# Kernel optimization log

Hardware: AMD Instinct MI355X
Metric: run time of the kernel (lower is better)

## Reference

```python
import jax, jax.numpy as jnp
import numpy as np

EPS = 1e-5
SLOPE = 0.2


def setup_inputs() -> dict:
    key = jax.random.key(0)
    ks = jax.random.split(key, 8)
    B, D, N = 8, 60, 1024
    dims = [(64, 120), (64, 64), (128, 64), (256, 128), (256, 512), (1024, 256)]
    inp = {"x": jax.random.normal(ks[0], (B, D, N), dtype=jnp.float32)}
    for i, (o, c) in enumerate(dims, 1):
        inp[f"w{i}"] = jax.random.normal(ks[i], (o, c), dtype=jnp.float32) / np.sqrt(c).astype(np.float32)
        inp[f"b{i}"] = jnp.zeros((o,), jnp.float32)
        inp[f"g{i}"] = jnp.ones((o,), jnp.float32)
        inp[f"be{i}"] = jnp.zeros((o,), jnp.float32)
    inp["k"] = 20
    return inp


def knn_idx(x, k):
    # x: [B, D, N] -> idx [B, N, k] of nearest neighbors (negative sq dist topk)
    inner = -2.0 * jnp.einsum('bdn,bdm->bnm', x, x)
    xx = jnp.sum(x * x, axis=1)  # [B, N]
    pd = -xx[:, :, None] - inner - xx[:, None, :]
    _, idx = jax.lax.top_k(pd, k)
    return idx


def get_graph_feature(x, k):
    # x: [B, D, N] -> [B, 2D, N, k]
    B, D, N = x.shape
    idx = knn_idx(x, k)  # [B, N, k]
    xt = jnp.transpose(x, (0, 2, 1))  # [B, N, D]
    nbr = xt[jnp.arange(B)[:, None, None], idx]  # [B, N, k, D]
    ctr = xt[:, :, None, :]  # [B, N, 1, D]
    feat = jnp.concatenate([nbr - ctr, jnp.broadcast_to(ctr, nbr.shape)], axis=-1)
    return jnp.transpose(feat, (0, 3, 1, 2))  # [B, 2D, N, k]


def lrelu(x):
    return jnp.where(x >= 0, x, SLOPE * x)


def bn(x, g, b, axes):
    # training-mode batch norm (biased variance), channel axis = 1
    m = jnp.mean(x, axis=axes, keepdims=True)
    v = jnp.mean((x - m) ** 2, axis=axes, keepdims=True)
    sh = [1] * x.ndim
    sh[1] = -1
    return (x - m) * jax.lax.rsqrt(v + EPS) * g.reshape(sh) + b.reshape(sh)


def conv2d1x1(x, w, b):
    return jnp.einsum('bcnk,oc->bonk', x, w) + b[None, :, None, None]


def conv1d1x1(x, w, b):
    return jnp.einsum('bcn,oc->bon', x, w) + b[None, :, None]


def reference(x, w1, b1, g1, be1, w2, b2, g2, be2, w3, b3, g3, be3,
              w4, b4, g4, be4, w5, b5, g5, be5, w6, b6, g6, be6, k):
    h = get_graph_feature(x, k)                             # [B,120,N,k]
    h = lrelu(bn(conv2d1x1(h, w1, b1), g1, be1, (0, 2, 3)))
    x1 = jnp.max(h, axis=-1)
    h = lrelu(bn(conv2d1x1(h, w2, b2), g2, be2, (0, 2, 3)))
    x2 = jnp.max(h, axis=-1)
    h = lrelu(bn(conv2d1x1(h, w3, b3), g3, be3, (0, 2, 3)))
    x3 = jnp.max(h, axis=-1)
    h = lrelu(bn(conv2d1x1(h, w4, b4), g4, be4, (0, 2, 3)))
    x4 = jnp.max(h, axis=-1)
    h = jnp.concatenate([x1, x2, x3, x4], axis=1)           # [B,512,N]
    h = lrelu(bn(conv1d1x1(h, w5, b5), g5, be5, (0, 2)))
    h = lrelu(bn(conv1d1x1(h, w6, b6), g6, be6, (0, 2)))
    return jnp.transpose(h, (0, 2, 1))                      # [B,N,emb_dims]
```

## Files before the change

### kernel.cpp

```cpp
#include <hip/hip_runtime.h>
#include <hip/hip_bf16.h>
#include <math.h>

#define B_ 8
#define D_ 60
#define N_ 1024
#define K_ 20
#define P1_ 8192
#define P2_ 163840

typedef __attribute__((ext_vector_type(8))) short bf16x8;
typedef __attribute__((ext_vector_type(4))) short bf16x4;
typedef __attribute__((ext_vector_type(4))) float f32x4;

__device__ inline float b2f(short s) { return __uint_as_float(((unsigned)(unsigned short)s) << 16); }
__device__ inline short f2b(float f) { __hip_bfloat16 h = __float2bfloat16(f); return *(short*)&h; }
__device__ inline unsigned fenc(float f) { unsigned b = __float_as_uint(f); return (b & 0x80000000u) ? ~b : (b | 0x80000000u); }
__device__ inline float fdec(unsigned k) { return __uint_as_float((k & 0x80000000u) ? (k ^ 0x80000000u) : ~k); }

#define OFF_IDX   0ull
#define OFF_XX    655360ull
#define OFF_STATS 688128ull
#define OFF_XT    720896ull
#define OFF_WB    1769472ull
#define OFF_XC    2662400ull
#define OFF_H5    11051008ull
#define OFF_H6    15245312ull
#define OFF_UV    32022528ull
#define OFF_XR1   36216832ull
#define OFF_XR2   38313984ull
#define OFF_XR3   40411136ull
#define OFF_XR4   44605440ull
#define OFF_H1    52994048ull
#define OFF_H2    73965568ull
#define OFF_H3    94937088ull
#define OFF_PART  136880128ull
#define OFF_PART2 139501568ull

#define WO1 0
#define WO2 8192
#define WO3 12288
#define WO4 20480
#define WO5 53248
#define WO6 184320

#define SO1 0
#define SO2 64
#define SO3 128
#define SO4 256
#define SO5 512
#define SO6 768
#define NCH_TOT 1792

__global__ __launch_bounds__(256) void k_xx(const float* __restrict__ x,
                                            float* __restrict__ xx) {
  int bn = blockIdx.x * 256 + threadIdx.x;
  int b = bn >> 10, n = bn & 1023;
  const float* xb = x + (size_t)b * D_ * N_ + n;
  float s = 0.f;
  for (int d = 0; d < D_; ++d) { float v = xb[(size_t)d * N_]; s += v * v; }
  xx[bn] = s;
}

__global__ __launch_bounds__(256) void k_pd(const float* __restrict__ x,
                                            const float* __restrict__ xx,
                                            float* __restrict__ pd) {
  __shared__ float lnn[D_][64];
  __shared__ float lmm[D_][128];
  int tid = threadIdx.x;
  int m0 = blockIdx.x * 128, n0 = blockIdx.y * 64, b = blockIdx.z;
  const float* xb = x + (size_t)b * D_ * N_;
  #pragma unroll
  for (int i = 0; i < 15; ++i) {
    int idx = tid + i * 256;
    int d = idx >> 6, col = idx & 63;
    lnn[d][col] = xb[(size_t)d * N_ + n0 + col];
  }
  #pragma unroll
  for (int i = 0; i < 30; ++i) {
    int idx = tid + i * 256;
    int d = idx >> 7, col = idx & 127;
    lmm[d][col] = xb[(size_t)d * N_ + m0 + col];
  }
  __syncthreads();
  int tn = tid >> 5, tm = tid & 31;
  float acc[8][4];
  #pragma unroll
  for (int i = 0; i < 8; ++i)
    #pragma unroll
    for (int j = 0; j < 4; ++j) acc[i][j] = 0.f;
  for (int d = 0; d < D_; ++d) {
    f32x4 mv  = *(const f32x4*)&lmm[d][tm * 4];
    f32x4 nva = *(const f32x4*)&lnn[d][tn * 8];
    f32x4 nvb = *(const f32x4*)&lnn[d][tn * 8 + 4];
    #pragma unroll
    for (int i = 0; i < 4; ++i)
      #pragma unroll
      for (int j = 0; j < 4; ++j) {
        acc[i][j]     = fmaf(nva[i], mv[j], acc[i][j]);
        acc[4 + i][j] = fmaf(nvb[i], mv[j], acc[4 + i][j]);
      }
  }
  const float* xxb = xx + b * 1024;
  f32x4 xxm = *(const f32x4*)(xxb + m0 + tm * 4);
  #pragma unroll
  for (int i = 0; i < 8; ++i) {
    int n = n0 + tn * 8 + i;
    float xxn = xxb[n];
    f32x4 o;
    #pragma unroll
    for (int j = 0; j < 4; ++j) o[j] = 2.f * acc[i][j] - xxn - xxm[j];
    *(f32x4*)(pd + ((size_t)(b * 1024 + n) * 1024) + m0 + tm * 4) = o;
  }
}

__global__ __launch_bounds__(256) void k_sel(const float* __restrict__ pd,
                                             int* __restrict__ idxb) {
  int tid = threadIdx.x;
  int wave = tid >> 6, lane = tid & 63;
  int bn = blockIdx.x * 4 + wave;
  const float* row = pd + (size_t)bn * 1024;
  int mbase = lane * 16;
  f32x4 r0 = *(const f32x4*)(row + mbase);
  f32x4 r1 = *(const f32x4*)(row + mbase + 4);
  f32x4 r2 = *(const f32x4*)(row + mbase + 8);
  f32x4 r3 = *(const f32x4*)(row + mbase + 12);
  float v[16];
  #pragma unroll
  for (int j = 0; j < 4; ++j) { v[j] = r0[j]; v[4 + j] = r1[j]; v[8 + j] = r2[j]; v[12 + j] = r3[j]; }
  int* outp = idxb + (size_t)bn * K_;
  for (int kk = 0; kk < K_; ++kk) {
    float bv = v[0]; int bj = 0;
    #pragma unroll
    for (int j = 1; j < 16; ++j)
      if (v[j] > bv) { bv = v[j]; bj = j; }
    int bi = mbase + bj;
    #pragma unroll
    for (int off = 1; off < 64; off <<= 1) {
      float ov = __shfl_xor(bv, off);
      int   oi = __shfl_xor(bi, off);
      if (ov > bv || (ov == bv && oi < bi)) { bv = ov; bi = oi; }
    }
    if (lane == 0) outp[kk] = bi;
    #pragma unroll
    for (int j = 0; j < 16; ++j)
      if (bi == mbase + j) v[j] = -INFINITY;
  }
}

__global__ __launch_bounds__(256) void k_xt(const float* __restrict__ x,
                                            short* __restrict__ xt) {
  int bn = blockIdx.x * 256 + threadIdx.x;
  int b = bn >> 10, n = bn & 1023;
  const float* xb = x + (size_t)b * D_ * N_ + n;
  short* row = xt + (size_t)bn * 64;
  for (int c = 0; c < 60; ++c) row[c] = f2b(xb[(size_t)c * N_]);
  row[60] = 0; row[61] = 0; row[62] = 0; row[63] = 0;
}

__global__ __launch_bounds__(256) void k_wuv(const float* __restrict__ w1,
                                             const float* __restrict__ b1,
                                             short* __restrict__ wuv,
                                             float* __restrict__ buv) {
  int t = blockIdx.x * 256 + threadIdx.x;
  int o = t >> 6, c = t & 63;
  float v = 0.f;
  if (o < 64) { if (c < 60) v = w1[o * 120 + c]; }
  else { int o2 = o - 64; if (c < 60) v = w1[o2 * 120 + 60 + c] - w1[o2 * 120 + c]; }
  wuv[t] = f2b(v);
  if (t < 128) buv[t] = (t < 64) ? 0.f : b1[t - 64];
}

__global__ __launch_bounds__(256) void k_wcvt(const float* __restrict__ w2,
                                              const float* __restrict__ w3,
                                              const float* __restrict__ w4,
                                              const float* __restrict__ w5,
                                              const float* __restrict__ w6,
                                              short* __restrict__ wbase) {
  int t = blockIdx.x * 256 + threadIdx.x;
  if (t < 4096) wbase[WO2 + t] = f2b(w2[t]);
  else if (t < 12288) wbase[WO3 + (t - 4096)] = f2b(w3[t - 4096]);
  else if (t < 45056) wbase[WO4 + (t - 12288)] = f2b(w4[t - 12288]);
  else if (t < 176128) wbase[WO5 + (t - 45056)] = f2b(w5[t - 45056]);
  else if (t < 438272) wbase[WO6 + (t - 176128)] = f2b(w6[t - 176128]);
}

template <int K, int COUT, bool APPLY, bool STATS, bool WMAX, bool HSTORE, bool F32OUT>
__global__ __launch_bounds__(256) void k_gemm(const short* __restrict__ in,
                                              const short* __restrict__ wb,
                                              const float* __restrict__ bias,
                                              const float* __restrict__ Ain,
                                              const float* __restrict__ Bin,
                                              float* __restrict__ part,
                                              short* __restrict__ out,
                                              unsigned* __restrict__ umax) {
  constexpr int KT = K / 32;
  constexpr int NX = COUT / 64;
  constexpr int MSZ = WMAX ? 128 * 68 : 4;
  __shared__ __align__(16) float m32s[MSZ];
  __shared__ float ls[128];
  int tid = threadIdx.x;
  int w = tid >> 6, lane = tid & 63;
  int ln = lane & 15, quad = lane >> 4;
  int bid = blockIdx.y * NX + blockIdx.x;
  int tot = NX * gridDim.y;
  int gid = (bid & 7) * (tot >> 3) + (bid >> 3);
  int bxx = gid % NX;
  int rp = gid / NX;
  int co0 = bxx * 64;
  const short* pA0 = in + ((size_t)(rp * 128 + w * 32 + ln)) * K + quad * 8;
  const short* pA1 = pA0 + (size_t)16 * K;
  const short* pW  = wb + ((size_t)(co0 + ln)) * K + quad * 8;

  f32x4 acc[4][2];
  #pragma unroll
  for (int m = 0; m < 4; ++m)
    #pragma unroll
    for (int t = 0; t < 2; ++t) acc[m][t] = (f32x4){0.f, 0.f, 0.f, 0.f};

  auto applyv = [&](bf16x8 v, int kc) -> bf16x8 {
    f32x4 a0 = *(const f32x4*)(Ain + kc);
    f32x4 a1 = *(const f32x4*)(Ain + kc + 4);
    f32x4 b0 = *(const f32x4*)(Bin + kc);
    f32x4 b1 = *(const f32x4*)(Bin + kc + 4);
    #pragma unroll
    for (int j = 0; j < 8; ++j) {
      float aj = j < 4 ? a0[j] : a1[j - 4];
      float bj = j < 4 ? b0[j] : b1[j - 4];
      float f = b2f(v[j]) * aj + bj;
      f = f >= 0.f ? f : 0.2f * f;
      v[j] = f2b(f);
    }
    return v;
  };

  bf16x8 wf0[4], wf1[4], af0[2], af1[2];
  #pragma unroll
  for (int m = 0; m < 4; ++m) wf0[m] = *(const bf16x8*)(pW + (size_t)m * 16 * K);
  af0[0] = *(const bf16x8*)(pA0);
  af0[1] = *(const bf16x8*)(pA1);
  if (APPLY) { af0[0] = applyv(af0[0], quad * 8); af0[1] = applyv(af0[1], quad * 8); }

  for (int kt = 0; kt < KT; kt += 2) {
    {
      int off = (kt + 1) * 32;
      #pragma unroll
      for (int m = 0; m < 4; ++m) wf1[m] = *(const bf16x8*)(pW + (size_t)m * 16 * K + off);
      af1[0] = *(const bf16x8*)(pA0 + off);
      af1[1] = *(const bf16x8*)(pA1 + off);
      if (APPLY) { af1[0] = applyv(af1[0], off + quad * 8); af1[1] = applyv(af1[1], off + quad * 8); }
    }
    #pragma unroll
    for (int m = 0; m < 4; ++m) {
      acc[m][0] = __builtin_amdgcn_mfma_f32_16x16x32_bf16(wf0[m], af0[0], acc[m][0], 0, 0, 0);
      acc[m][1] = __builtin_amdgcn_mfma_f32_16x16x32_bf16(wf0[m], af0[1], acc[m][1], 0, 0, 0);
    }
    if (kt + 2 < KT) {
      int off = (kt + 2) * 32;
      #pragma unroll
      for (int m = 0; m < 4; ++m) wf0[m] = *(const bf16x8*)(pW + (size_t)m * 16 * K + off);
      af0[0] = *(const bf16x8*)(pA0 + off);
      af0[1] = *(const bf16x8*)(pA1 + off);
      if (APPLY) { af0[0] = applyv(af0[0], off + quad * 8); af0[1] = applyv(af0[1], off + quad * 8); }
    }
    #pragma unroll
    for (int m = 0; m < 4; ++m) {
      acc[m][0] = __builtin_amdgcn_mfma_f32_16x16x32_bf16(wf1[m], af1[0], acc[m][0], 0, 0, 0);
      acc[m][1] = __builtin_amdgcn_mfma_f32_16x16x32_bf16(wf1[m], af1[1], acc[m][1], 0, 0, 0);
    }
  }

  #pragma unroll
  for (int m = 0; m < 4; ++m) {
    f32x4 bs = *(const f32x4*)(bias + co0 + m * 16 + quad * 4);
    #pragma unroll
    for (int t = 0; t < 2; ++t)
      #pragma unroll
      for (int r = 0; r < 4; ++r) acc[m][t][r] += bs[r];
  }
  if (HSTORE) {
    #pragma unroll
    for (int m = 0; m < 4; ++m)
      #pragma unroll
      for (int t = 0; t < 2; ++t) {
        int p = rp * 128 + w * 32 + t * 16 + ln;
        if (F32OUT) {
          *(f32x4*)((float*)out + (size_t)p * COUT + co0 + m * 16 + quad * 4) = acc[m][t];
        } else {
          bf16x4 o;
          #pragma unroll
          for (int r = 0; r < 4; ++r) o[r] = f2b(acc[m][t][r]);
          *(bf16x4*)(out + (size_t)p * COUT + co0 + m * 16 + quad * 4) = o;
        }
      }
  }
  if (STATS || WMAX) {
    if (STATS && tid < 128) ls[tid] = 0.f;
    if (WMAX) {
      #pragma unroll
      for (int m = 0; m < 4; ++m)
        #pragma unroll
        for (int t = 0; t < 2; ++t)
          *(f32x4*)(m32s + (size_t)(w * 32 + t * 16 + ln) * 68 + m * 16 + quad * 4) = acc[m][t];
    }
    __syncthreads();
    if (STATS) {
      #pragma unroll
      for (int m = 0; m < 4; ++m)
        #pragma unroll
        for (int r = 0; r < 4; ++r) {
          float v0 = acc[m][0][r], v1 = acc[m][1][r];
          float s = v0 + v1, ss = v0 * v0 + v1 * v1;
          #pragma unroll
          for (int off = 1; off < 16; off <<= 1) {
            s += __shfl_xor(s, off); ss += __shfl_xor(ss, off);
          }
          if (ln == 0) {
            atomicAdd(&ls[m * 16 + quad * 4 + r], s);
            atomicAdd(&ls[64 + m * 16 + quad * 4 + r], ss);
          }
        }
    }
    if (WMAX) {
      int r0 = rp * 128;
      int pt0 = r0 / 20;
      int npt = (r0 + 127) / 20 - pt0 + 1;
      if (tid < npt * 16) {
        int lpt = tid >> 4, cq = (tid & 15) * 4;
        int ptg = pt0 + lpt;
        int rs = ptg * 20 - r0, re = rs + 20;
        rs = rs < 0 ? 0 : rs;
        re = re > 128 ? 128 : re;
        f32x4 mv = (f32x4){-INFINITY, -INFINITY, -INFINITY, -INFINITY};
        for (int r = rs; r < re; ++r) {
          f32x4 v = *(const f32x4*)(m32s + (size_t)r * 68 + cq);
          #pragma unroll
          for (int j = 0; j < 4; ++j) mv[j] = fmaxf(mv[j], v[j]);
        }
        #pragma unroll
        for (int j = 0; j < 4; ++j)
          atomicMax(&umax[(size_t)ptg * COUT + co0 + cq + j], fenc(mv[j]));
      }
    }
  }
  if (STATS) {
    __syncthreads();
    if (tid < 128)
      part[((size_t)bxx * gridDim.y + rp) * 128 + tid] = ls[tid];
  }
}

__global__ __launch_bounds__(256) void k_expand(const float* __restrict__ UVf,
                                                const int* __restrict__ idxb,
                                                short* __restrict__ h1,
                                                float* __restrict__ xr1,
                                                float* __restrict__ part) {
  int tid = threadIdx.x;
  int lp = tid >> 4;
  int c0 = (tid & 15) * 4;
  int pt = blockIdx.x * 16 + lp;
  int base = (pt >> 10) << 10;
  f32x4 V = *(const f32x4*)(UVf + (size_t)pt * 128 + 64 + c0);
  f32x4 sum = (f32x4){0.f, 0.f, 0.f, 0.f};
  f32x4 ssq = (f32x4){0.f, 0.f, 0.f, 0.f};
  f32x4 mx = (f32x4){-INFINITY, -INFINITY, -INFINITY, -INFINITY};
  const int* ip = idxb + (size_t)pt * K_;
  size_t hb = (size_t)pt * K_ * 64 + c0;
  for (int k = 0; k < K_; ++k) {
    int nb = base + ip[k];
    f32x4 U = *(const f32x4*)(UVf + (size_t)nb * 128 + c0);
    bf16x4 o;
    #pragma unroll
    for (int j = 0; j < 4; ++j) {
      float h = U[j] + V[j];
      mx[j] = fmaxf(mx[j], U[j]);
      sum[j] += h; ssq[j] += h * h;
      o[j] = f2b(h);
    }
    *(bf16x4*)(h1 + hb + (size_t)k * 64) = o;
  }
  f32x4 xo;
  #pragma unroll
  for (int j = 0; j < 4; ++j) xo[j] = mx[j] + V[j];
  *(f32x4*)(xr1 + (size_t)pt * 64 + c0) = xo;
  __shared__ float ls[2048];
  *(f32x4*)(ls + tid * 4) = sum;
  *(f32x4*)(ls + 1024 + tid * 4) = ssq;
  __syncthreads();
  if (tid < 32) {
    int cl = tid & 15;
    bool issq = tid >= 16;
    const float* src = ls + (issq ? 1024 : 0);
    f32x4 s = (f32x4){0.f, 0.f, 0.f, 0.f};
    #pragma unroll
    for (int g = 0; g < 16; ++g) {
      f32x4 v = *(const f32x4*)(src + (g * 16 + cl) * 4);
      s[0] += v[0]; s[1] += v[1]; s[2] += v[2]; s[3] += v[3];
    }
    *(f32x4*)(part + (size_t)blockIdx.x * 128 + (issq ? 64 : 0) + cl * 4) = s;
  }
}

__global__ __launch_bounds__(256) void k_red(const float* __restrict__ part, int NB,
                                             float* __restrict__ part2) {
  int cc = blockIdx.x, by = blockIdx.y;
  int tid = threadIdx.x;
  int rg = tid >> 5;
  int c4 = (tid & 31) * 4;
  int chunk = NB >> 5;
  const float* p = part + ((size_t)cc * NB + (size_t)by * chunk) * 128;
  f32x4 acc = (f32x4){0.f, 0.f, 0.f, 0.f};
  for (int r = rg; r < chunk; r += 8) {
    f32x4 v = *(const f32x4*)(p + (size_t)r * 128 + c4);
    acc[0] += v[0]; acc[1] += v[1]; acc[2] += v[2]; acc[3] += v[3];
  }
  __shared__ float lds[1024];
  *(f32x4*)(lds + tid * 4) = acc;
  __syncthreads();
  if (tid < 32) {
    f32x4 s = (f32x4){0.f, 0.f, 0.f, 0.f};
    #pragma unroll
    for (int g = 0; g < 8; ++g) {
      f32x4 v = *(const f32x4*)(lds + (g * 32 + tid) * 4);
      s[0] += v[0]; s[1] += v[1]; s[2] += v[2]; s[3] += v[3];
    }
    *(f32x4*)(part2 + ((size_t)cc * 32 + by) * 128 + tid * 4) = s;
  }
}

__global__ __launch_bounds__(256) void k_bnab(const float* __restrict__ part, int NB,
                                              const float* __restrict__ g,
                                              const float* __restrict__ be,
                                              float* __restrict__ A,
                                              float* __restrict__ Bp, float inv) {
  __shared__ float red[256];
  int tid = threadIdx.x;
  int j = tid & 127, h = tid >> 7;
  const float* p = part + (size_t)blockIdx.x * NB * 128;
  float s = 0.f;
  for (int bx = h; bx < NB; bx += 2) s += p[(size_t)bx * 128 + j];
  red[tid] = s;
  __syncthreads();
  if (tid < 128) red[tid] = red[tid] + red[tid + 128];
  __syncthreads();
  if (tid < 64) {
    int c = blockIdx.x * 64 + tid;
    float m = red[tid] * inv;
    float v = red[64 + tid] * inv - m * m;
    float a = g[c] * rsqrtf(v + 1e-5f);
    A[c] = a; Bp[c] = be[c] - m * a;
  }
}

__global__ __launch_bounds__(256) void k_xcat(const float* __restrict__ xr1,
                                              const unsigned* __restrict__ xr2,
                                              const unsigned* __restrict__ xr3,
                                              const unsigned* __restrict__ xr4,
                                              const float* __restrict__ A,
                                              const float* __restrict__ Bp,
                                              short* __restrict__ xcat) {
  int t = blockIdx.x * 256 + threadIdx.x;
  int p = t >> 7, cq = t & 127;
  int c0 = cq * 4;
  f32x4 v;
  if (c0 < 64) {
    v = *(const f32x4*)(xr1 + (size_t)p * 64 + c0);
  } else {
    const unsigned* src; int cc;
    if (c0 < 128)      { src = xr2 + (size_t)p * 64;  cc = c0 - 64; }
    else if (c0 < 256) { src = xr3 + (size_t)p * 128; cc = c0 - 128; }
    else               { src = xr4 + (size_t)p * 256; cc = c0 - 256; }
    #pragma unroll
    for (int j = 0; j < 4; ++j) v[j] = fdec(src[cc + j]);
  }
  f32x4 a = *(const f32x4*)(A + c0);
  f32x4 b = *(const f32x4*)(Bp + c0);
  bf16x4 o;
  #pragma unroll
  for (int j = 0; j < 4; ++j) {
    float f = v[j] * a[j] + b[j];
    f = f >= 0.f ? f : 0.2f * f;
    o[j] = f2b(f);
  }
  *(bf16x4*)(xcat + (size_t)p * 512 + c0) = o;
}

__global__ __launch_bounds__(256) void k_apply_out(const short* __restrict__ h,
                                                   const float* __restrict__ A,
                                                   const float* __restrict__ Bp,
                                                   float* __restrict__ out) {
  int t = blockIdx.x * 256 + threadIdx.x;
  int c0 = (t & 255) * 4;
  f32x4 a = *(const f32x4*)(A + c0);
  f32x4 b = *(const f32x4*)(Bp + c0);
  bf16x4 v = *(const bf16x4*)(h + (size_t)t * 4);
  f32x4 o;
  #pragma unroll
  for (int r = 0; r < 4; ++r) {
    float f = b2f(v[r]) * a[r] + b[r];
    o[r] = f >= 0.f ? f : 0.2f * f;
  }
  *(f32x4*)(out + (size_t)t * 4) = o;
}

extern "C" void kernel_launch(void* const* d_in, const int* in_sizes, int n_in,
                              void* d_out, int out_size, void* d_ws, size_t ws_size,
                              hipStream_t stream) {
  const float* x   = (const float*)d_in[0];
  const float* w1  = (const float*)d_in[1];
  const float* b1  = (const float*)d_in[2];
  const float* g1  = (const float*)d_in[3];
  const float* be1 = (const float*)d_in[4];
  const float* w2  = (const float*)d_in[5];
  const float* b2  = (const float*)d_in[6];
  const float* g2  = (const float*)d_in[7];
  const float* be2 = (const float*)d_in[8];
  const float* w3  = (const float*)d_in[9];
  const float* b3  = (const float*)d_in[10];
  const float* g3  = (const float*)d_in[11];
  const float* be3 = (const float*)d_in[12];
  const float* w4  = (const float*)d_in[13];
  const float* b4  = (const float*)d_in[14];
  const float* g4  = (const float*)d_in[15];
  const float* be4 = (const float*)d_in[16];
  const float* w5  = (const float*)d_in[17];
  const float* b5  = (const float*)d_in[18];
  const float* g5  = (const float*)d_in[19];
  const float* be5 = (const float*)d_in[20];
  const float* w6  = (const float*)d_in[21];
  const float* b6  = (const float*)d_in[22];
  const float* g6  = (const float*)d_in[23];
  const float* be6 = (const float*)d_in[24];
  float* out = (float*)d_out;
  char* ws = (char*)d_ws;

  int*      idxb = (int*)(ws + OFF_IDX);
  float*    xx   = (float*)(ws + OFF_XX);
  float*    Aall = (float*)(ws + OFF_STATS);
  float*    Ball = Aall + NCH_TOT;
  float*    buv  = Ball + NCH_TOT;
  short*    xt   = (short*)(ws + OFF_XT);
  short*    wbb  = (short*)(ws + OFF_WB);
  short*    xcat = (short*)(ws + OFF_XC);
  short*    h5   = (short*)(ws + OFF_H5);
  short*    h6   = (short*)(ws + OFF_H6);
  float*    UVf  = (float*)(ws + OFF_UV);
  float*    xr1  = (float*)(ws + OFF_XR1);
  unsigned* xr2  = (unsigned*)(ws + OFF_XR2);
  unsigned* xr3  = (unsigned*)(ws + OFF_XR3);
  unsigned* xr4  = (unsigned*)(ws + OFF_XR4);
  short*    h1   = (short*)(ws + OFF_H1);
  short*    h2   = (short*)(ws + OFF_H2);
  short*    h3   = (short*)(ws + OFF_H3);
  float*    pd    = (float*)(ws + OFF_H3);
  float*    part  = (float*)(ws + OFF_PART);
  float*    part2 = (float*)(ws + OFF_PART2);

  hipMemsetAsync(ws + OFF_XR2, 0, 2097152ull + 4194304ull + 8388608ull, stream);

  k_xx <<<P1_ / 256, 256, 0, stream>>>(x, xx);
  k_pd <<<dim3(8, 16, 8), 256, 0, stream>>>(x, xx, pd);
  k_sel<<<P1_ / 4, 256, 0, stream>>>(pd, idxb);
  k_xt <<<P1_ / 256, 256, 0, stream>>>(x, xt);
  k_wuv<<<32, 256, 0, stream>>>(w1, b1, wbb + WO1, buv);
  k_wcvt<<<1712, 256, 0, stream>>>(w2, w3, w4, w5, w6, wbb);

  k_gemm<64, 128, false, false, false, true, true><<<dim3(2, 64), 256, 0, stream>>>(
      xt, wbb + WO1, buv, nullptr, nullptr, nullptr, (short*)UVf, nullptr);
  k_expand<<<P1_ / 16, 256, 0, stream>>>(UVf, idxb, h1, xr1, part);
  k_red <<<dim3(1, 32), 256, 0, stream>>>(part, P1_ / 16, part2);
  k_bnab<<<1, 256, 0, stream>>>(part2, 32, g1, be1, Aall + SO1, Ball + SO1, 1.f / P2_);

  k_gemm<64, 64, true, true, true, true, false><<<dim3(1, P2_ / 128), 256, 0, stream>>>(
      h1, wbb + WO2, b2, Aall + SO1, Ball + SO1, part, h2, xr2);
  k_red <<<dim3(1, 32), 256, 0, stream>>>(part, P2_ / 128, part2);
  k_bnab<<<1, 256, 0, stream>>>(part2, 32, g2, be2, Aall + SO2, Ball + SO2, 1.f / P2_);

  k_gemm<64, 128, true, true, true, true, false><<<dim3(2, P2_ / 128), 256, 0, stream>>>(
      h2, wbb + WO3, b3, Aall + SO2, Ball + SO2, part, h3, xr3);
  k_red <<<dim3(2, 32), 256, 0, stream>>>(part, P2_ / 128, part2);
  k_bnab<<<2, 256, 0, stream>>>(part2, 32, g3, be3, Aall + SO3, Ball + SO3, 1.f / P2_);

  k_gemm<128, 256, true, true, true, false, false><<<dim3(4, P2_ / 128), 256, 0, stream>>>(
      h3, wbb + WO4, b4, Aall + SO3, Ball + SO3, part, nullptr, xr4);
  k_red <<<dim3(4, 32), 256, 0, stream>>>(part, P2_ / 128, part2);
  k_bnab<<<4, 256, 0, stream>>>(part2, 32, g4, be4, Aall + SO4, Ball + SO4, 1.f / P2_);

  k_xcat<<<P1_ * 128 / 256, 256, 0, stream>>>(xr1, xr2, xr3, xr4, Aall, Ball, xcat);

  k_gemm<512, 256, false, true, false, true, false><<<dim3(4, P1_ / 128), 256, 0, stream>>>(
      xcat, wbb + WO5, b5, nullptr, nullptr, part, h5, nullptr);
  k_bnab<<<4, 256, 0, stream>>>(part, P1_ / 128, g5, be5, Aall + SO5, Ball + SO5, 1.f / P1_);

  k_gemm<256, 1024, true, true, false, true, false><<<dim3(16, P1_ / 128), 256, 0, stream>>>(
      h5, wbb + WO6, b6, Aall + SO5, Ball + SO5, part, h6, nullptr);
  k_bnab<<<16, 256, 0, stream>>>(part, P1_ / 128, g6, be6, Aall + SO6, Ball + SO6, 1.f / P1_);
  k_apply_out<<<P1_ * 256 / 256, 256, 0, stream>>>(h6, Aall + SO6, Ball + SO6, out);

  (void)in_sizes; (void)n_in; (void)out_size; (void)ws_size;
}
```

Before: 477.6 us.

## Stage GEMM tiles through swizzled LDS with async global_load_lds double buffering

Rewrites the MFMA GEMM so operand tiles are copied into XOR-swizzled shared memory with global_load_lds and double buffered. Each block now handles several 128-row tiles (NR) to amortise weight loads and launch count. Per-channel stats are reduced with wave shuffles and written per wave instead of through shared-memory atomics. The neighbour max is done with shuffle-based segmented reduction and global atomicMax instead of a shared-memory staging buffer. This changes the partial-sum counts and the workspace offset, and it adds a barrier on every K-step.

```diff
diff --git a/kernel.cpp b/kernel.cpp
--- a/kernel.cpp
+++ b/kernel.cpp
@@ -17,6 +17,12 @@
 __device__ inline short f2b(float f) { __hip_bfloat16 h = __float2bfloat16(f); return *(short*)&h; }
 __device__ inline unsigned fenc(float f) { unsigned b = __float_as_uint(f); return (b & 0x80000000u) ? ~b : (b | 0x80000000u); }
 __device__ inline float fdec(unsigned k) { return __uint_as_float((k & 0x80000000u) ? (k ^ 0x80000000u) : ~k); }
+
+__device__ __forceinline__ void gl16(const short* g, short* l) {
+  __builtin_amdgcn_global_load_lds(
+      (const __attribute__((address_space(1))) unsigned int*)g,
+      (__attribute__((address_space(3))) unsigned int*)l, 16, 0, 0);
+}
 
 #define OFF_IDX   0ull
 #define OFF_XX    655360ull
@@ -35,7 +41,7 @@
 #define OFF_H2    73965568ull
 #define OFF_H3    94937088ull
 #define OFF_PART  136880128ull
-#define OFF_PART2 139501568ull
+#define OFF_PART2 149463040ull
 
 #define WO1 0
 #define WO2 8192
@@ -185,7 +191,7 @@
   else if (t < 438272) wbase[WO6 + (t - 176128)] = f2b(w6[t - 176128]);
 }
 
-template <int K, int COUT, bool APPLY, bool STATS, bool WMAX, bool HSTORE, bool F32OUT>
+template <int K, int COUT, int NR, bool APPLY, bool STATS, bool WMAX, bool HSTORE, bool F32OUT>
 __global__ __launch_bounds__(256) void k_gemm(const short* __restrict__ in,
                                               const short* __restrict__ wb,
                                               const float* __restrict__ bias,
@@ -194,29 +200,43 @@
                                               float* __restrict__ part,
                                               short* __restrict__ out,
                                               unsigned* __restrict__ umax) {
-  constexpr int KT = K / 32;
-  constexpr int NX = COUT / 64;
-  constexpr int MSZ = WMAX ? 128 * 68 : 4;
-  __shared__ __align__(16) float m32s[MSZ];
-  __shared__ float ls[128];
+  constexpr int NKP = K / 64;
+  constexpr int NP  = NR * NKP;
+  constexpr int ASZ = 128 * 64;
+  constexpr int WSZ = 64 * 64;
+  __shared__ __align__(16) short ldsA[2 * ASZ];
+  __shared__ __align__(16) short ldsW[2 * WSZ];
+
   int tid = threadIdx.x;
   int w = tid >> 6, lane = tid & 63;
   int ln = lane & 15, quad = lane >> 4;
-  int bid = blockIdx.y * NX + blockIdx.x;
-  int tot = NX * gridDim.y;
+  int xsl = ln & 7;
+  int bid = blockIdx.y * gridDim.x + blockIdx.x;
+  int tot = gridDim.x * gridDim.y;
   int gid = (bid & 7) * (tot >> 3) + (bid >> 3);
-  int bxx = gid % NX;
-  int rp = gid / NX;
+  int bxx = gid % gridDim.x;
+  int rpB = gid / gridDim.x;
   int co0 = bxx * 64;
-  const short* pA0 = in + ((size_t)(rp * 128 + w * 32 + ln)) * K + quad * 8;
-  const short* pA1 = pA0 + (size_t)16 * K;
-  const short* pW  = wb + ((size_t)(co0 + ln)) * K + quad * 8;
-
-  f32x4 acc[4][2];
-  #pragma unroll
-  for (int m = 0; m < 4; ++m)
-    #pragma unroll
-    for (int t = 0; t < 2; ++t) acc[m][t] = (f32x4){0.f, 0.f, 0.f, 0.f};
+
+  const int rl = lane >> 3;
+  const int c16 = (lane & 7) ^ (rl & 7);
+
+  auto stage = [&](int p, int b) {
+    const int rp_ = rpB * NR + p / NKP;
+    const int kp_ = p % NKP;
+    const short* sA = in + (size_t)(rp_ * 128) * K + kp_ * 64;
+    #pragma unroll
+    for (int i = 0; i < 4; ++i) {
+      int ch = w * 4 + i;
+      gl16(sA + (size_t)(ch * 8 + rl) * K + c16 * 8, ldsA + b * ASZ + ch * 512);
+    }
+    const short* sW = wb + (size_t)co0 * K + kp_ * 64;
+    #pragma unroll
+    for (int i = 0; i < 2; ++i) {
+      int ch = w * 2 + i;
+      gl16(sW + (size_t)(ch * 8 + rl) * K + c16 * 8, ldsW + b * WSZ + ch * 512);
+    }
+  };
 
   auto applyv = [&](bf16x8 v, int kc) -> bf16x8 {
     f32x4 a0 = *(const f32x4*)(Ain + kc);
@@ -234,119 +254,120 @@
     return v;
   };
 
-  bf16x8 wf0[4], wf1[4], af0[2], af1[2];
-  #pragma unroll
-  for (int m = 0; m < 4; ++m) wf0[m] = *(const bf16x8*)(pW + (size_t)m * 16 * K);
-  af0[0] = *(const bf16x8*)(pA0);
-  af0[1] = *(const bf16x8*)(pA1);
-  if (APPLY) { af0[0] = applyv(af0[0], quad * 8); af0[1] = applyv(af0[1], quad * 8); }
-
-  for (int kt = 0; kt < KT; kt += 2) {
-    {
-      int off = (kt + 1) * 32;
+  f32x4 acc[4][2];
+  float sacc[4][4], ssacc[4][4];
+  #pragma unroll
+  for (int m = 0; m < 4; ++m)
+    #pragma unroll
+    for (int j = 0; j < 4; ++j) { sacc[m][j] = 0.f; ssacc[m][j] = 0.f; }
+
+  stage(0, 0);
+  __syncthreads();
+
+  for (int p = 0; p < NP; ++p) {
+    const int b = p & 1;
+    if (p + 1 < NP) stage(p + 1, b ^ 1);
+    const int rp_ = rpB * NR + p / NKP;
+    const int kp_ = p % NKP;
+    if (kp_ == 0) {
       #pragma unroll
-      for (int m = 0; m < 4; ++m) wf1[m] = *(const bf16x8*)(pW + (size_t)m * 16 * K + off);
-      af1[0] = *(const bf16x8*)(pA0 + off);
-      af1[1] = *(const bf16x8*)(pA1 + off);
-      if (APPLY) { af1[0] = applyv(af1[0], off + quad * 8); af1[1] = applyv(af1[1], off + quad * 8); }
-    }
-    #pragma unroll
-    for (int m = 0; m < 4; ++m) {
-      acc[m][0] = __builtin_amdgcn_mfma_f32_16x16x32_bf16(wf0[m], af0[0], acc[m][0], 0, 0, 0);
-      acc[m][1] = __builtin_amdgcn_mfma_f32_16x16x32_bf16(wf0[m], af0[1], acc[m][1], 0, 0, 0);
-    }
-    if (kt + 2 < KT) {
-      int off = (kt + 2) * 32;
+      for (int m = 0; m < 4; ++m)
+        #pragma unroll
+        for (int t = 0; t < 2; ++t) acc[m][t] = (f32x4){0.f, 0.f, 0.f, 0.f};
+    }
+    #pragma unroll
+    for (int ks = 0; ks < 2; ++ks) {
+      bf16x8 fw[4], fa[2];
+      int sl = ((ks * 4 + quad) ^ xsl) * 8;
       #pragma unroll
-      for (int m = 0; m < 4; ++m) wf0[m] = *(const bf16x8*)(pW + (size_t)m * 16 * K + off);
-      af0[0] = *(const bf16x8*)(pA0 + off);
-      af0[1] = *(const bf16x8*)(pA1 + off);
-      if (APPLY) { af0[0] = applyv(af0[0], off + quad * 8); af0[1] = applyv(af0[1], off + quad * 8); }
-    }
-    #pragma unroll
-    for (int m = 0; m < 4; ++m) {
-      acc[m][0] = __builtin_amdgcn_mfma_f32_16x16x32_bf16(wf1[m], af1[0], acc[m][0], 0, 0, 0);
-      acc[m][1] = __builtin_amdgcn_mfma_f32_16x16x32_bf16(wf1[m], af1[1], acc[m][1], 0, 0, 0);
-    }
-  }
-
-  #pragma unroll
-  for (int m = 0; m < 4; ++m) {
-    f32x4 bs = *(const f32x4*)(bias + co0 + m * 16 + quad * 4);
-    #pragma unroll
-    for (int t = 0; t < 2; ++t)
-      #pragma unroll
-      for (int r = 0; r < 4; ++r) acc[m][t][r] += bs[r];
-  }
-  if (HSTORE) {
-    #pragma unroll
-    for (int m = 0; m < 4; ++m)
+      for (int m = 0; m < 4; ++m)
+        fw[m] = *(const bf16x8*)(ldsW + b * WSZ + (m * 16 + ln) * 64 + sl);
       #pragma unroll
       for (int t = 0; t < 2; ++t) {
-        int p = rp * 128 + w * 32 + t * 16 + ln;
-        if (F32OUT) {
-          *(f32x4*)((float*)out + (size_t)p * COUT + co0 + m * 16 + quad * 4) = acc[m][t];
-        } else {
-          bf16x4 o;
-          #pragma unroll
-          for (int r = 0; r < 4; ++r) o[r] = f2b(acc[m][t][r]);
-          *(bf16x4*)(out + (size_t)p * COUT + co0 + m * 16 + quad * 4) = o;
-        }
+        fa[t] = *(const bf16x8*)(ldsA + b * ASZ + (w * 32 + t * 16 + ln) * 64 + sl);
+        if (APPLY) fa[t] = applyv(fa[t], kp_ * 64 + ks * 32 + quad * 8);
       }
-  }
-  if (STATS || WMAX) {
-    if (STATS && tid < 128) ls[tid] = 0.f;
-    if (WMAX) {
       #pragma unroll
       for (int m = 0; m < 4; ++m)
         #pragma unroll
         for (int t = 0; t < 2; ++t)
-          *(f32x4*)(m32s + (size_t)(w * 32 + t * 16 + ln) * 68 + m * 16 + quad * 4) = acc[m][t];
+          acc[m][t] = __builtin_amdgcn_mfma_f32_16x16x32_bf16(fw[m], fa[t], acc[m][t], 0, 0, 0);
+    }
+    if (kp_ == NKP - 1) {
+      #pragma unroll
+      for (int m = 0; m < 4; ++m) {
+        f32x4 bs = *(const f32x4*)(bias + co0 + m * 16 + quad * 4);
+        #pragma unroll
+        for (int t = 0; t < 2; ++t)
+          #pragma unroll
+          for (int j = 0; j < 4; ++j) acc[m][t][j] += bs[j];
+      }
+      const int prow = rp_ * 128 + w * 32;
+      if (HSTORE) {
+        #pragma unroll
+        for (int m = 0; m < 4; ++m)
+          #pragma unroll
+          for (int t = 0; t < 2; ++t) {
+            int pp_ = prow + t * 16 + ln;
+            if (F32OUT) {
+              *(f32x4*)((float*)out + (size_t)pp_ * COUT + co0 + m * 16 + quad * 4) = acc[m][t];
+            } else {
+              bf16x4 o;
+              #pragma unroll
+              for (int jr = 0; jr < 4; ++jr) o[jr] = f2b(acc[m][t][jr]);
+              *(bf16x4*)(out + (size_t)pp_ * COUT + co0 + m * 16 + quad * 4) = o;
+            }
+          }
+      }
+      if (STATS) {
+        #pragma unroll
+        for (int m = 0; m < 4; ++m)
+          #pragma unroll
+          for (int j = 0; j < 4; ++j) {
+            float v0 = acc[m][0][j], v1 = acc[m][1][j];
+            float s = v0 + v1, ss = v0 * v0 + v1 * v1;
+            #pragma unroll
+            for (int off = 1; off < 16; off <<= 1) {
+              s += __shfl_xor(s, off); ss += __shfl_xor(ss, off);
+            }
+            sacc[m][j] += s; ssacc[m][j] += ss;
+          }
+      }
+      if (WMAX) {
+        #pragma unroll
+        for (int t = 0; t < 2; ++t) {
+          int row = prow + t * 16 + ln;
+          int g = row / 20;
+          bool lead = (ln == 0) || (row - g * 20 == 0);
+          int og1 = __shfl_xor(g, 1), og2 = __shfl_xor(g, 2);
+          int og4 = __shfl_xor(g, 4), og8 = __shfl_xor(g, 8);
+          #pragma unroll
+          for (int m = 0; m < 4; ++m)
+            #pragma unroll
+            for (int j = 0; j < 4; ++j) {
+              float v = acc[m][t][j];
+              float ov;
+              ov = __shfl_xor(v, 1); if (og1 == g && ov > v) v = ov;
+              ov = __shfl_xor(v, 2); if (og2 == g && ov > v) v = ov;
+              ov = __shfl_xor(v, 4); if (og4 == g && ov > v) v = ov;
+              ov = __shfl_xor(v, 8); if (og8 == g && ov > v) v = ov;
+              if (lead) atomicMax(&umax[(size_t)g * COUT + co0 + m * 16 + quad * 4 + j], fenc(v));
+            }
+        }
+      }
     }
     __syncthreads();
-    if (STATS) {
+  }
+  if (STATS && ln == 0) {
+    size_t key = ((size_t)bxx * gridDim.y + rpB) * 4 + w;
+    float* pp = part + key * 128;
+    #pragma unroll
+    for (int m = 0; m < 4; ++m)
       #pragma unroll
-      for (int m = 0; m < 4; ++m)
-        #pragma unroll
-        for (int r = 0; r < 4; ++r) {
-          float v0 = acc[m][0][r], v1 = acc[m][1][r];
-          float s = v0 + v1, ss = v0 * v0 + v1 * v1;
-          #pragma unroll
-          for (int off = 1; off < 16; off <<= 1) {
-            s += __shfl_xor(s, off); ss += __shfl_xor(ss, off);
-          }
-          if (ln == 0) {
-            atomicAdd(&ls[m * 16 + quad * 4 + r], s);
-            atomicAdd(&ls[64 + m * 16 + quad * 4 + r], ss);
-          }
-        }
-    }
-    if (WMAX) {
-      int r0 = rp * 128;
-      int pt0 = r0 / 20;
-      int npt = (r0 + 127) / 20 - pt0 + 1;
-      if (tid < npt * 16) {
-        int lpt = tid >> 4, cq = (tid & 15) * 4;
-        int ptg = pt0 + lpt;
-        int rs = ptg * 20 - r0, re = rs + 20;
-        rs = rs < 0 ? 0 : rs;
-        re = re > 128 ? 128 : re;
-        f32x4 mv = (f32x4){-INFINITY, -INFINITY, -INFINITY, -INFINITY};
-        for (int r = rs; r < re; ++r) {
-          f32x4 v = *(const f32x4*)(m32s + (size_t)r * 68 + cq);
-          #pragma unroll
-          for (int j = 0; j < 4; ++j) mv[j] = fmaxf(mv[j], v[j]);
-        }
-        #pragma unroll
-        for (int j = 0; j < 4; ++j)
-          atomicMax(&umax[(size_t)ptg * COUT + co0 + cq + j], fenc(mv[j]));
+      for (int j = 0; j < 4; ++j) {
+        pp[m * 16 + quad * 4 + j] = sacc[m][j];
+        pp[64 + m * 16 + quad * 4 + j] = ssacc[m][j];
       }
-    }
-  }
-  if (STATS) {
-    __syncthreads();
-    if (tid < 128)
-      part[((size_t)bxx * gridDim.y + rp) * 128 + tid] = ls[tid];
   }
 }
 
@@ -565,36 +586,36 @@
   k_wuv<<<32, 256, 0, stream>>>(w1, b1, wbb + WO1, buv);
   k_wcvt<<<1712, 256, 0, stream>>>(w2, w3, w4, w5, w6, wbb);
 
-  k_gemm<64, 128, false, false, false, true, true><<<dim3(2, 64), 256, 0, stream>>>(
+  k_gemm<64, 128, 1, false, false, false, true, true><<<dim3(2, 64), 256, 0, stream>>>(
       xt, wbb + WO1, buv, nullptr, nullptr, nullptr, (short*)UVf, nullptr);
   k_expand<<<P1_ / 16, 256, 0, stream>>>(UVf, idxb, h1, xr1, part);
   k_red <<<dim3(1, 32), 256, 0, stream>>>(part, P1_ / 16, part2);
   k_bnab<<<1, 256, 0, stream>>>(part2, 32, g1, be1, Aall + SO1, Ball + SO1, 1.f / P2_);
 
-  k_gemm<64, 64, true, true, true, true, false><<<dim3(1, P2_ / 128), 256, 0, stream>>>(
+  k_gemm<64, 64, 2, true, true, true, true, false><<<dim3(1, 640), 256, 0, stream>>>(
       h1, wbb + WO2, b2, Aall + SO1, Ball + SO1, part, h2, xr2);
-  k_red <<<dim3(1, 32), 256, 0, stream>>>(part, P2_ / 128, part2);
+  k_red <<<dim3(1, 32), 256, 0, stream>>>(part, 2560, part2);
   k_bnab<<<1, 256, 0, stream>>>(part2, 32, g2, be2, Aall + SO2, Ball + SO2, 1.f / P2_);
 
-  k_gemm<64, 128, true, true, true, true, false><<<dim3(2, P2_ / 128), 256, 0, stream>>>(
+  k_gemm<64, 128, 2, true, true, true, true, false><<<dim3(2, 640), 256, 0, stream>>>(
       h2, wbb + WO3, b3, Aall + SO2, Ball + SO2, part, h3, xr3);
-  k_red <<<dim3(2, 32), 256, 0, stream>>>(part, P2_ / 128, part2);
+  k_red <<<dim3(2, 32), 256, 0, stream>>>(part, 2560, part2);
   k_bnab<<<2, 256, 0, stream>>>(part2, 32, g3, be3, Aall + SO3, Ball + SO3, 1.f / P2_);
 
-  k_gemm<128, 256, true, true, true, false, false><<<dim3(4, P2_ / 128), 256, 0, stream>>>(
+  k_gemm<128, 256, 4, true, true, true, false, false><<<dim3(4, 320), 256, 0, stream>>>(
       h3, wbb + WO4, b4, Aall + SO3, Ball + SO3, part, nullptr, xr4);
-  k_red <<<dim3(4, 32), 256, 0, stream>>>(part, P2_ / 128, part2);
+  k_red <<<dim3(4, 32), 256, 0, stream>>>(part, 1280, part2);
   k_bnab<<<4, 256, 0, stream>>>(part2, 32, g4, be4, Aall + SO4, Ball + SO4, 1.f / P2_);
 
   k_xcat<<<P1_ * 128 / 256, 256, 0, stream>>>(xr1, xr2, xr3, xr4, Aall, Ball, xcat);
 
-  k_gemm<512, 256, false, true, false, true, false><<<dim3(4, P1_ / 128), 256, 0, stream>>>(
+  k_gemm<512, 256, 1, false, true, false, true, false><<<dim3(4, 64), 256, 0, stream>>>(
       xcat, wbb + WO5, b5, nullptr, nullptr, part, h5, nullptr);
-  k_bnab<<<4, 256, 0, stream>>>(part, P1_ / 128, g5, be5, Aall + SO5, Ball + SO5, 1.f / P1_);
-
-  k_gemm<256, 1024, true, true, false, true, false><<<dim3(16, P1_ / 128), 256, 0, stream>>>(
+  k_bnab<<<4, 256, 0, stream>>>(part, 256, g5, be5, Aall + SO5, Ball + SO5, 1.f / P1_);
+
+  k_gemm<256, 1024, 1, true, true, false, true, false><<<dim3(16, 64), 256, 0, stream>>>(
       h5, wbb + WO6, b6, Aall + SO5, Ball + SO5, part, h6, nullptr);
-  k_bnab<<<16, 256, 0, stream>>>(part, P1_ / 128, g6, be6, Aall + SO6, Ball + SO6, 1.f / P1_);
+  k_bnab<<<16, 256, 0, stream>>>(part, 256, g6, be6, Aall + SO6, Ball + SO6, 1.f / P1_);
   k_apply_out<<<P1_ * 256 / 256, 256, 0, stream>>>(h6, Aall + SO6, Ball + SO6, out);
 
   (void)in_sizes; (void)n_in; (void)out_size; (void)ws_size;
```

New measurement: 583.0 us. 22.1% more time.
